# Optimization experiments

Measured on AMD Instinct MI355X. Metric: run time of the kernel, lower is better.

## Reference

```python
import jax, jax.numpy as jnp
import numpy as np

D_KEY = 128
INF = 1e9  # stands in for the module's global INF constant


def setup_inputs() -> dict:
    key = jax.random.key(0)
    kq, kk, kv = jax.random.split(key, 3)
    B, S, D = 8, 4096, D_KEY
    return {
        "query": jax.random.normal(kq, (B, S, D), dtype=jnp.float32),
        "keys": jax.random.normal(kk, (B, S, D), dtype=jnp.float32),
        "values": jax.random.normal(kv, (B, S, D), dtype=jnp.float32),
    }


def reference(query, keys, values):
    # dot_products: [B, Sq, Sk]
    scores = jnp.einsum("bqd,bkd->bqk", query, keys)
    S = scores.shape[-1]
    # causal: subtract INF on strict upper triangle (triu(1)), applied BEFORE scaling
    causal = jnp.triu(jnp.ones((S, S), dtype=scores.dtype), 1) * INF
    logits = (scores - causal[None, :, :]) / jnp.asarray(np.sqrt(D_KEY), scores.dtype)
    # legacy F.softmax on 3D transposed tensor == softmax over key axis
    probs = jax.nn.softmax(logits, axis=-1)
    # dropout with p=0.0 is identity
    return jnp.einsum("bqk,bkd->bqd", probs, values)
```

## Files before the change

### kernel.cpp

```cpp
#include <hip/hip_runtime.h>

#define B_SZ   8
#define S_LEN  4096
#define D_K    128
#define KB     64
#define CH     16
#define NCHUNK 1280

#define PT_STR 72

typedef short  short8  __attribute__((ext_vector_type(8)));
typedef float  floatx4 __attribute__((ext_vector_type(4)));

#define EXP2F(x) exp2f(x)

__device__ __forceinline__ unsigned bfround(float x) {
  unsigned u = __builtin_bit_cast(unsigned, x);
  return (u + 0x7fffu + ((u >> 16) & 1u)) >> 16;
}
__device__ __forceinline__ unsigned bfpack2(float a, float b) {
  return bfround(a) | (bfround(b) << 16);
}
__device__ __forceinline__ unsigned cvtpk(float lo, float hi) {
  unsigned r;
  asm("v_cvt_pk_bf16_f32 %0, %1, %2" : "=v"(r) : "v"(lo), "v"(hi));
  return r;
}

__device__ __forceinline__ void dma16(const void* g, const void* l) {
  __builtin_amdgcn_global_load_lds(
      (__attribute__((address_space(1))) unsigned int*)(unsigned long long)g,
      (__attribute__((address_space(3))) unsigned int*)(unsigned int)(unsigned long long)l,
      16, 0, 0);
}


__global__ __launch_bounds__(256)
void prep(const float* __restrict__ K, const float* __restrict__ V,
          unsigned short* __restrict__ Kb, unsigned short* __restrict__ Vt) {
  __shared__ float tile[64][129];
  const int tid = threadIdx.x;
  const int bid = blockIdx.x;
  const int b   = bid >> 6;
  const int s   = bid & 63;
  const int kt  = s * 64;

  {
    const int r  = tid >> 2;
    const int cq = tid & 3;
    const float* kp = K + (size_t)(b * S_LEN + kt + r) * D_K + cq * 32;
    unsigned short* kdst = Kb + (size_t)bid * 8192 + r * 128;
    const int xr = (r & 7) << 4;
#pragma unroll
    for (int j = 0; j < 4; ++j) {
      float4 f0 = *(const float4*)(kp + j * 8);
      float4 f1 = *(const float4*)(kp + j * 8 + 4);
      uint4 u;
      u.x = bfpack2(f0.x, f0.y);
      u.y = bfpack2(f0.z, f0.w);
      u.z = bfpack2(f1.x, f1.y);
      u.w = bfpack2(f1.z, f1.w);
      const int o = (cq * 64 + j * 16) ^ xr;
      *(uint4*)(kdst + (o >> 1)) = u;
    }
  }

  {
    const int k  = tid >> 2;
    const int cq = tid & 3;
    const float* vp = V + (size_t)(b * S_LEN + kt + k) * D_K + cq * 32;
#pragma unroll
    for (int i = 0; i < 8; ++i) {
      float4 f = *(const float4*)(vp + i * 4);
      tile[k][cq * 32 + i * 4]     = f.x;
      tile[k][cq * 32 + i * 4 + 1] = f.y;
      tile[k][cq * 32 + i * 4 + 2] = f.z;
      tile[k][cq * 32 + i * 4 + 3] = f.w;
    }
  }
  __syncthreads();

  {
    const int d = tid >> 1;
    const int h = tid & 1;
    unsigned short* vdst = Vt + (size_t)bid * 8192 + d * 64;
    const int xr = (d & 7) << 4;
#pragma unroll
    for (int j = 0; j < 4; ++j) {
      const int k0 = h * 32 + j * 8;
      uint4 u;
      u.x = bfpack2(tile[k0 + 0][d], tile[k0 + 1][d]);
      u.y = bfpack2(tile[k0 + 2][d], tile[k0 + 3][d]);
      u.z = bfpack2(tile[k0 + 4][d], tile[k0 + 5][d]);
      u.w = bfpack2(tile[k0 + 6][d], tile[k0 + 7][d]);
      const int o = (h * 64 + j * 16) ^ xr;
      *(uint4*)(vdst + (o >> 1)) = u;
    }
  }
}

__global__ void zero_cnt(int* cnt) { *cnt = 0; }


__global__ __launch_bounds__(128, 2)
void attn_worker(const float* __restrict__ Q, const unsigned short* __restrict__ Kb,
                 const unsigned short* __restrict__ Vt, int* __restrict__ cnt,
                 float* __restrict__ ml, float* __restrict__ pO) {
  __shared__ __align__(16) short Klds[2][8192];
  __shared__ __align__(16) short Vtlds[2][8192];
  __shared__ __align__(16) short Plds[2 * 16 * PT_STR];
  __shared__ int s_chunk;

  const int tid  = threadIdx.x;
  const int lane = tid & 63;
  const int w    = tid >> 6;
  const int l15  = lane & 15;
  const int quad = lane >> 4;
  const int xk   = (l15 & 7) << 3;

  const float CSC = 0.12752041f;

  for (;;) {
    if (tid == 0) s_chunk = atomicAdd(cnt, 1);
    __syncthreads();
    const int c = s_chunk;
    if (c >= NCHUNK) break;

    int b, qi, j;
    if (c < 800) {
      const int r = c >> 3;  b = c & 7;
      if      (r <  4) { qi = 63;               j = r;            }
      else if (r < 52) { qi = 62 - (r-4)/3;     j = (r-4)%3;      }
      else if (r < 84) { qi = 46 - (r-52)/2;    j = (r-52)%2;     }
      else             { qi = 30 - (r-84);      j = 0;            }
    } else {
      const int rc = c - 800;
      const int s  = 15 - (rc >> 5);
      const int t  = rc & 31;
      b  = t & 7;
      qi = s - 1 + 16 * (t >> 3);
      j  = (qi + 1) >> 4;
    }

    const int q0 = qi * 64;
    const int s0 = j * CH;
    const int s1 = min(s0 + CH, qi + 1);

    short8 bq[2][4];
    int qg[2];
#pragma unroll
    for (int sub = 0; sub < 2; ++sub) {
      qg[sub] = q0 + w * 32 + sub * 16 + l15;
      const float* qrow = Q + (size_t)(b * S_LEN + qg[sub]) * D_K + quad * 8;
#pragma unroll
      for (int kd = 0; kd < 4; ++kd) {
        float4 f0 = *(const float4*)(qrow + kd * 32);
        float4 f1 = *(const float4*)(qrow + kd * 32 + 4);
        union { short8 s; unsigned u[4]; } t;
        t.u[0] = bfpack2(f0.x, f0.y);
        t.u[1] = bfpack2(f0.z, f0.w);
        t.u[2] = bfpack2(f1.x, f1.y);
        t.u[3] = bfpack2(f1.z, f1.w);
        bq[sub][kd] = t.s;
      }
    }

    floatx4 acc[2][8];
#pragma unroll
    for (int sub = 0; sub < 2; ++sub)
#pragma unroll
      for (int nc = 0; nc < 8; ++nc) acc[sub][nc] = (floatx4){0.f, 0.f, 0.f, 0.f};
    float m_run[2] = {-1e30f, -1e30f}, l_run[2] = {0.f, 0.f};

    const unsigned short* kb0 = Kb + (size_t)b * 64 * 8192;
    const unsigned short* vb0 = Vt + (size_t)b * 64 * 8192;
    const int lo = lane * 8;

#define STAGE(BUF, S)                                                          \
    do {                                                                       \
      const unsigned short* kg_ = kb0 + (size_t)(S) * 8192 + w * 4096 + lo;    \
      const unsigned short* vg_ = vb0 + (size_t)(S) * 8192 + w * 4096 + lo;    \
      short* kl_ = &Klds[BUF][w * 4096];                                       \
      short* vl_ = &Vtlds[BUF][w * 4096];                                      \
      _Pragma("unroll")                                                        \
      for (int i_ = 0; i_ < 8; ++i_) dma16(kg_ + i_ * 512, kl_ + i_ * 512);    \
      _Pragma("unroll")                                                        \
      for (int i_ = 0; i_ < 8; ++i_) dma16(vg_ + i_ * 512, vl_ + i_ * 512);    \
    } while (0)

    STAGE(s0 & 1, s0);
    if (s0 + 1 < s1) {
      STAGE((s0 + 1) & 1, s0 + 1);
      asm volatile("s_waitcnt vmcnt(16)" ::: "memory");
    } else {
      asm volatile("s_waitcnt vmcnt(0)" ::: "memory");
    }
    __builtin_amdgcn_s_barrier();
    __builtin_amdgcn_sched_barrier(0);

    for (int s = s0; s < s1; ++s) {
      const int kt  = s * KB;
      const int cur = s & 1;
      const short* Kl = &Klds[cur][0];
      const short* Vl = &Vtlds[cur][0];

      floatx4 st[2][4];
#pragma unroll
      for (int kf = 0; kf < 4; ++kf) {
        floatx4 c0 = (floatx4){0.f, 0.f, 0.f, 0.f};
        floatx4 c1 = (floatx4){0.f, 0.f, 0.f, 0.f};
#pragma unroll
        for (int kd = 0; kd < 4; ++kd) {
          short8 a = *(const short8*)(&Kl[((kf * 16 + l15) << 7) + ((kd * 32 + quad * 8) ^ xk)]);
          c0 = __builtin_amdgcn_mfma_f32_16x16x32_bf16(a, bq[0][kd], c0, 0, 0, 0);
          c1 = __builtin_amdgcn_mfma_f32_16x16x32_bf16(a, bq[1][kd], c1, 0, 0, 0);
        }
        st[0][kf] = c0;
        st[1][kf] = c1;
      }

      if (s == qi) {
#pragma unroll
        for (int sub = 0; sub < 2; ++sub)
#pragma unroll
          for (int kf = 0; kf < 4; ++kf)
#pragma unroll
            for (int r = 0; r < 4; ++r) {
              int key = kt + kf * 16 + quad * 4 + r;
              if (key > qg[sub]) st[sub][kf][r] = -1e30f;
            }
      }

      short8 pa[2][2];
#pragma unroll
      for (int sub = 0; sub < 2; ++sub) {
        float mx = st[sub][0][0];
#pragma unroll
        for (int kf = 0; kf < 4; ++kf)
#pragma unroll
          for (int r = 0; r < 4; ++r) mx = fmaxf(mx, st[sub][kf][r]);
        mx = fmaxf(mx, __shfl_xor(mx, 16, 64));
        mx = fmaxf(mx, __shfl_xor(mx, 32, 64));
        const float m_new = fmaxf(m_run[sub], mx);
        const float alpha = EXP2F((m_run[sub] - m_new) * CSC);

        float p[4][4];
        float tsum = 0.f;
#pragma unroll
        for (int kf = 0; kf < 4; ++kf)
#pragma unroll
          for (int r = 0; r < 4; ++r) {
            p[kf][r] = EXP2F((st[sub][kf][r] - m_new) * CSC);
            tsum += p[kf][r];
          }
        tsum += __shfl_xor(tsum, 16, 64);
        tsum += __shfl_xor(tsum, 32, 64);
        l_run[sub] = l_run[sub] * alpha + tsum;
        m_run[sub] = m_new;

#pragma unroll
        for (int r = 0; r < 4; ++r) {
          const float ar = __shfl(alpha, quad * 4 + r, 64);
#pragma unroll
          for (int nc = 0; nc < 8; ++nc) acc[sub][nc][r] *= ar;
        }

        short* pw = &Plds[(w * 16 + l15) * PT_STR];
#pragma unroll
        for (int kf = 0; kf < 4; ++kf) {
          uint2 u;
          u.x = cvtpk(p[kf][0], p[kf][1]);
          u.y = cvtpk(p[kf][2], p[kf][3]);
          *(uint2*)(&pw[kf * 16 + quad * 4]) = u;
        }
        __asm__ __volatile__("" ::: "memory");
        pa[sub][0] = *(const short8*)(&pw[quad * 8]);
        pa[sub][1] = *(const short8*)(&pw[32 + quad * 8]);
        __asm__ __volatile__("" ::: "memory");
      }

#pragma unroll
      for (int nc = 0; nc < 8; ++nc) {
        short8 bv0 = *(const short8*)(&Vl[((nc * 16 + l15) << 6) + ((quad * 8) ^ xk)]);
        short8 bv1 = *(const short8*)(&Vl[((nc * 16 + l15) << 6) + ((32 + quad * 8) ^ xk)]);
        acc[0][nc] = __builtin_amdgcn_mfma_f32_16x16x32_bf16(pa[0][0], bv0, acc[0][nc], 0, 0, 0);
        acc[0][nc] = __builtin_amdgcn_mfma_f32_16x16x32_bf16(pa[0][1], bv1, acc[0][nc], 0, 0, 0);
        acc[1][nc] = __builtin_amdgcn_mfma_f32_16x16x32_bf16(pa[1][0], bv0, acc[1][nc], 0, 0, 0);
        acc[1][nc] = __builtin_amdgcn_mfma_f32_16x16x32_bf16(pa[1][1], bv1, acc[1][nc], 0, 0, 0);
      }

      asm volatile("s_waitcnt lgkmcnt(0)" ::: "memory");
      __builtin_amdgcn_s_barrier();
      __builtin_amdgcn_sched_barrier(0);
      if (s + 2 < s1) {
        STAGE(cur, s + 2);
        asm volatile("s_waitcnt vmcnt(16)" ::: "memory");
      } else if (s + 1 < s1) {
        asm volatile("s_waitcnt vmcnt(0)" ::: "memory");
      }
      __builtin_amdgcn_s_barrier();
      __builtin_amdgcn_sched_barrier(0);
    }
#undef STAGE

    const int slot = ((b << 6) | qi) * 4 + j;
    float* po = pO + (size_t)slot * 8192;
#pragma unroll
    for (int sub = 0; sub < 2; ++sub) {
#pragma unroll
      for (int r = 0; r < 4; ++r) {
        const int qrow = w * 32 + sub * 16 + quad * 4 + r;
        float* op = po + qrow * D_K + l15;
#pragma unroll
        for (int nc = 0; nc < 8; ++nc) op[nc * 16] = acc[sub][nc][r];
      }
      if (quad == 0) {
        const int qrow = w * 32 + sub * 16 + l15;
        ml[(size_t)slot * 128 + qrow * 2]     = m_run[sub];
        ml[(size_t)slot * 128 + qrow * 2 + 1] = l_run[sub];
      }
    }
  }
}


__global__ __launch_bounds__(256)
void attn_combine(const float* __restrict__ ml, const float* __restrict__ pO,
                  float* __restrict__ O) {
  const int t   = blockIdx.x;
  const int b   = t >> 6;
  const int qi  = t & 63;
  const int ncb = ((qi + 1) + 15) >> 4;
  const float CSC = 0.12752041f;

  const int tid = threadIdx.x;
  const int q   = tid >> 2;
  const int dp  = (tid & 3) * 32;

  float m[4], l[4];
  float M = -1e30f;
  for (int jj = 0; jj < ncb; ++jj) {
    const int slot = t * 4 + jj;
    m[jj] = ml[(size_t)slot * 128 + q * 2];
    l[jj] = ml[(size_t)slot * 128 + q * 2 + 1];
    M = fmaxf(M, m[jj]);
  }
  float wgt[4], L = 0.f;
  for (int jj = 0; jj < ncb; ++jj) {
    wgt[jj] = EXP2F((m[jj] - M) * CSC);
    L += wgt[jj] * l[jj];
  }
  const float inv = 1.0f / L;

  float4 out[8];
#pragma unroll
  for (int v = 0; v < 8; ++v) out[v] = make_float4(0.f, 0.f, 0.f, 0.f);
  for (int jj = 0; jj < ncb; ++jj) {
    const float* src = pO + (size_t)(t * 4 + jj) * 8192 + q * D_K + dp;
    const float wj = wgt[jj];
#pragma unroll
    for (int v = 0; v < 8; ++v) {
      float4 f = *(const float4*)(src + v * 4);
      out[v].x += wj * f.x;  out[v].y += wj * f.y;
      out[v].z += wj * f.z;  out[v].w += wj * f.w;
    }
  }
  float* dst = O + (size_t)(b * S_LEN + qi * 64 + q) * D_K + dp;
#pragma unroll
  for (int v = 0; v < 8; ++v) {
    float4 f = make_float4(out[v].x * inv, out[v].y * inv, out[v].z * inv, out[v].w * inv);
    *(float4*)(dst + v * 4) = f;
  }
}


#define KT_STR 136
#define VT_STR 72

__global__ __launch_bounds__(256, 2)
void attn_fwd_fb(const float* __restrict__ Q, const float* __restrict__ K,
                 const float* __restrict__ V, float* __restrict__ O) {
  __shared__ __align__(16) short Klds[KB * KT_STR];
  __shared__ __align__(16) short Vtlds[D_K * VT_STR];
  __shared__ __align__(16) short Plds[4 * 16 * PT_STR];

  const int tid  = threadIdx.x;
  const int lane = tid & 63;
  const int w    = tid >> 6;
  const int l15  = lane & 15;
  const int quad = lane >> 4;

  const int bid = blockIdx.x;
  const int b   = bid & 7;
  const int qi  = 63 - (bid >> 3);
  const int q0  = qi * 64;

  const float CSC = 0.12752041f;

  const int    qg   = q0 + w * 16 + l15;
  const float* qrow = Q + (size_t)(b * S_LEN + qg) * D_K + quad * 8;
  short8 bq[4];
#pragma unroll
  for (int kd = 0; kd < 4; ++kd) {
    float4 f0 = *(const float4*)(qrow + kd * 32);
    float4 f1 = *(const float4*)(qrow + kd * 32 + 4);
    union { short8 s; unsigned u[4]; } t;
    t.u[0] = bfpack2(f0.x, f0.y);
    t.u[1] = bfpack2(f0.z, f0.w);
    t.u[2] = bfpack2(f1.x, f1.y);
    t.u[3] = bfpack2(f1.z, f1.w);
    bq[kd] = t.s;
  }

  floatx4 acc[8];
#pragma unroll
  for (int nc = 0; nc < 8; ++nc) acc[nc] = (floatx4){0.f, 0.f, 0.f, 0.f};
  float m_run = -1e30f, l_run = 0.f;

  const int d4 = tid & 31;
  const int kq = tid >> 5;
  const int nsteps = qi + 1;

  for (int s = 0; s < nsteps; ++s) {
    const int kt = s * KB;
#pragma unroll
    for (int r2 = 0; r2 < 2; ++r2) {
      const int row = r2 * 32 + kq * 4;
      const float* kp = K + (size_t)(b * S_LEN + kt + row) * D_K + d4 * 4;
      const float* vp = V + (size_t)(b * S_LEN + kt + row) * D_K + d4 * 4;
      float4 fk[4], fv[4];
#pragma unroll
      for (int i = 0; i < 4; ++i) {
        fk[i] = *(const float4*)(kp + i * D_K);
        fv[i] = *(const float4*)(vp + i * D_K);
      }
#pragma unroll
      for (int i = 0; i < 4; ++i) {
        uint2 u;
        u.x = bfpack2(fk[i].x, fk[i].y);
        u.y = bfpack2(fk[i].z, fk[i].w);
        *(uint2*)(&Klds[(row + i) * KT_STR + d4 * 4]) = u;
      }
#pragma unroll
      for (int c = 0; c < 4; ++c) {
        float e0 = ((const float*)&fv[0])[c];
        float e1 = ((const float*)&fv[1])[c];
        float e2 = ((const float*)&fv[2])[c];
        float e3 = ((const float*)&fv[3])[c];
        uint2 u;
        u.x = bfpack2(e0, e1);
        u.y = bfpack2(e2, e3);
        *(uint2*)(&Vtlds[(d4 * 4 + c) * VT_STR + row]) = u;
      }
    }
    __syncthreads();

    floatx4 st[4];
#pragma unroll
    for (int kf = 0; kf < 4; ++kf) {
      floatx4 c = (floatx4){0.f, 0.f, 0.f, 0.f};
#pragma unroll
      for (int kd = 0; kd < 4; ++kd) {
        short8 a = *(const short8*)(&Klds[(kf * 16 + l15) * KT_STR + kd * 32 + quad * 8]);
        c = __builtin_amdgcn_mfma_f32_16x16x32_bf16(a, bq[kd], c, 0, 0, 0);
      }
      st[kf] = c;
    }

    if (s == nsteps - 1) {
#pragma unroll
      for (int kf = 0; kf < 4; ++kf)
#pragma unroll
        for (int rr = 0; rr < 4; ++rr) {
          int key = kt + kf * 16 + quad * 4 + rr;
          if (key > qg) st[kf][rr] = -1e30f;
        }
    }

    float mx = st[0][0];
#pragma unroll
    for (int kf = 0; kf < 4; ++kf)
#pragma unroll
      for (int rr = 0; rr < 4; ++rr) mx = fmaxf(mx, st[kf][rr]);
    mx = fmaxf(mx, __shfl_xor(mx, 16, 64));
    mx = fmaxf(mx, __shfl_xor(mx, 32, 64));
    const float m_new = fmaxf(m_run, mx);
    const float alpha = EXP2F((m_run - m_new) * CSC);

    float p[4][4];
    float tsum = 0.f;
#pragma unroll
    for (int kf = 0; kf < 4; ++kf)
#pragma unroll
      for (int rr = 0; rr < 4; ++rr) {
        p[kf][rr] = EXP2F((st[kf][rr] - m_new) * CSC);
        tsum += p[kf][rr];
      }
    tsum += __shfl_xor(tsum, 16, 64);
    tsum += __shfl_xor(tsum, 32, 64);
    l_run = l_run * alpha + tsum;
    m_run = m_new;

#pragma unroll
    for (int rr = 0; rr < 4; ++rr) {
      const float ar = __shfl(alpha, quad * 4 + rr, 64);
#pragma unroll
      for (int nc = 0; nc < 8; ++nc) acc[nc][rr] *= ar;
    }

    short* pw = &Plds[(w * 16 + l15) * PT_STR];
#pragma unroll
    for (int kf = 0; kf < 4; ++kf) {
      uint2 u;
      u.x = bfpack2(p[kf][0], p[kf][1]);
      u.y = bfpack2(p[kf][2], p[kf][3]);
      *(uint2*)(&pw[kf * 16 + quad * 4]) = u;
    }
    __asm__ __volatile__("" ::: "memory");
    short8 pa0 = *(const short8*)(&pw[quad * 8]);
    short8 pa1 = *(const short8*)(&pw[32 + quad * 8]);

#pragma unroll
    for (int nc = 0; nc < 8; ++nc) {
      short8 bv0 = *(const short8*)(&Vtlds[(nc * 16 + l15) * VT_STR + quad * 8]);
      acc[nc] = __builtin_amdgcn_mfma_f32_16x16x32_bf16(pa0, bv0, acc[nc], 0, 0, 0);
      short8 bv1 = *(const short8*)(&Vtlds[(nc * 16 + l15) * VT_STR + 32 + quad * 8]);
      acc[nc] = __builtin_amdgcn_mfma_f32_16x16x32_bf16(pa1, bv1, acc[nc], 0, 0, 0);
    }
    __syncthreads();
  }

#pragma unroll
  for (int rr = 0; rr < 4; ++rr) {
    const float lr  = __shfl(l_run, quad * 4 + rr, 64);
    const float inv = 1.0f / lr;
    const int qout  = q0 + w * 16 + quad * 4 + rr;
    float* op = O + (size_t)(b * S_LEN + qout) * D_K + l15;
#pragma unroll
    for (int nc = 0; nc < 8; ++nc) op[nc * 16] = acc[nc][rr] * inv;
  }
}


extern "C" void kernel_launch(void* const* d_in, const int* in_sizes, int n_in,
                              void* d_out, int out_size, void* d_ws, size_t ws_size,
                              hipStream_t stream) {
  const float* Q = (const float*)d_in[0];
  const float* K = (const float*)d_in[1];
  const float* V = (const float*)d_in[2];
  float* O = (float*)d_out;

  const size_t elems = (size_t)B_SZ * S_LEN * D_K;

  const size_t off_ml = 256;
  const size_t off_po = off_ml + 2048ull * 128 * 4;
  const size_t off_kb = off_po + 2048ull * 8192 * 4;
  const size_t off_vt = off_kb + elems * 2;
  const size_t need   = off_vt + elems * 2;

  if (ws_size >= need) {
    char* ws = (char*)d_ws;
    int*            cnt = (int*)ws;
    float*          mlp = (float*)(ws + off_ml);
    float*          po  = (float*)(ws + off_po);
    unsigned short* Kbp = (unsigned short*)(ws + off_kb);
    unsigned short* Vtp = (unsigned short*)(ws + off_vt);

    zero_cnt<<<dim3(1), dim3(1), 0, stream>>>(cnt);
    prep<<<dim3(B_SZ * 64), dim3(256), 0, stream>>>(K, V, Kbp, Vtp);
    attn_worker<<<dim3(1024), dim3(128), 0, stream>>>(Q, Kbp, Vtp, cnt, mlp, po);
    attn_combine<<<dim3(512), dim3(256), 0, stream>>>(mlp, po, O);
  } else {
    attn_fwd_fb<<<dim3(512), dim3(256), 0, stream>>>(Q, K, V, O);
  }
}
```

Baseline: 217.7 us.

## Use 128-row query tiles with 4-wave workgroups sharing each K/V stage

Doubles the query tile per work chunk from 64 to 128 rows, with four waves per workgroup instead of two. Each staged K/V block in LDS now serves twice as many queries, which halves the number of chunks and the global-to-LDS traffic per query. Waves whose rows lie entirely before the current key block skip their compute, and the causal mask is applied per 16-row sub-block. The combine kernel and workspace layout are resized to match; the coarser tiles reduce load-balancing granularity and add more idle waves along the diagonal.

```diff
diff --git a/kernel.cpp b/kernel.cpp
--- a/kernel.cpp
+++ b/kernel.cpp
@@ -5,7 +5,7 @@
 #define D_K    128
 #define KB     64
 #define CH     16
-#define NCHUNK 1280
+#define NCHUNK 640
 
 #define PT_STR 72
 
@@ -52,15 +52,15 @@
     unsigned short* kdst = Kb + (size_t)bid * 8192 + r * 128;
     const int xr = (r & 7) << 4;
 #pragma unroll
-    for (int j = 0; j < 4; ++j) {
-      float4 f0 = *(const float4*)(kp + j * 8);
-      float4 f1 = *(const float4*)(kp + j * 8 + 4);
+    for (int jj = 0; jj < 4; ++jj) {
+      float4 f0 = *(const float4*)(kp + jj * 8);
+      float4 f1 = *(const float4*)(kp + jj * 8 + 4);
       uint4 u;
       u.x = bfpack2(f0.x, f0.y);
       u.y = bfpack2(f0.z, f0.w);
       u.z = bfpack2(f1.x, f1.y);
       u.w = bfpack2(f1.z, f1.w);
-      const int o = (cq * 64 + j * 16) ^ xr;
+      const int o = (cq * 64 + jj * 16) ^ xr;
       *(uint4*)(kdst + (o >> 1)) = u;
     }
   }
@@ -86,14 +86,14 @@
     unsigned short* vdst = Vt + (size_t)bid * 8192 + d * 64;
     const int xr = (d & 7) << 4;
 #pragma unroll
-    for (int j = 0; j < 4; ++j) {
-      const int k0 = h * 32 + j * 8;
+    for (int jj = 0; jj < 4; ++jj) {
+      const int k0 = h * 32 + jj * 8;
       uint4 u;
       u.x = bfpack2(tile[k0 + 0][d], tile[k0 + 1][d]);
       u.y = bfpack2(tile[k0 + 2][d], tile[k0 + 3][d]);
       u.z = bfpack2(tile[k0 + 4][d], tile[k0 + 5][d]);
       u.w = bfpack2(tile[k0 + 6][d], tile[k0 + 7][d]);
-      const int o = (h * 64 + j * 16) ^ xr;
+      const int o = (h * 64 + jj * 16) ^ xr;
       *(uint4*)(vdst + (o >> 1)) = u;
     }
   }
@@ -102,13 +102,13 @@
 __global__ void zero_cnt(int* cnt) { *cnt = 0; }
 
 
-__global__ __launch_bounds__(128, 2)
+__global__ __launch_bounds__(256, 2)
 void attn_worker(const float* __restrict__ Q, const unsigned short* __restrict__ Kb,
                  const unsigned short* __restrict__ Vt, int* __restrict__ cnt,
                  float* __restrict__ ml, float* __restrict__ pO) {
   __shared__ __align__(16) short Klds[2][8192];
   __shared__ __align__(16) short Vtlds[2][8192];
-  __shared__ __align__(16) short Plds[2 * 16 * PT_STR];
+  __shared__ __align__(16) short Plds[4 * 16 * PT_STR];
   __shared__ int s_chunk;
 
   const int tid  = threadIdx.x;
@@ -126,25 +126,25 @@
     const int c = s_chunk;
     if (c >= NCHUNK) break;
 
-    int b, qi, j;
-    if (c < 800) {
+    int b, q, j;
+    if (c < 416) {
       const int r = c >> 3;  b = c & 7;
-      if      (r <  4) { qi = 63;               j = r;            }
-      else if (r < 52) { qi = 62 - (r-4)/3;     j = (r-4)%3;      }
-      else if (r < 84) { qi = 46 - (r-52)/2;    j = (r-52)%2;     }
-      else             { qi = 30 - (r-84);      j = 0;            }
+      if      (r <  4) { q = 31;              j = r;         }
+      else if (r < 28) { q = 30 - (r-4)/3;    j = (r-4)%3;   }
+      else if (r < 44) { q = 22 - (r-28)/2;   j = (r-28)%2;  }
+      else             { q = 14 - (r-44);     j = 0;         }
     } else {
-      const int rc = c - 800;
-      const int s  = 15 - (rc >> 5);
+      const int rc = c - 416;
+      const int g  = rc >> 5;
       const int t  = rc & 31;
-      b  = t & 7;
-      qi = s - 1 + 16 * (t >> 3);
-      j  = (qi + 1) >> 4;
-    }
-
-    const int q0 = qi * 64;
+      b = t & 7;
+      q = (6 - g) + 8 * (3 - (t >> 3));
+      j = (q + 1) >> 3;
+    }
+
+    const int q0 = q * 128;
     const int s0 = j * CH;
-    const int s1 = min(s0 + CH, qi + 1);
+    const int s1 = min(s0 + CH, 2 * q + 2);
 
     short8 bq[2][4];
     int qg[2];
@@ -178,20 +178,20 @@
 
 #define STAGE(BUF, S)                                                          \
     do {                                                                       \
-      const unsigned short* kg_ = kb0 + (size_t)(S) * 8192 + w * 4096 + lo;    \
-      const unsigned short* vg_ = vb0 + (size_t)(S) * 8192 + w * 4096 + lo;    \
-      short* kl_ = &Klds[BUF][w * 4096];                                       \
-      short* vl_ = &Vtlds[BUF][w * 4096];                                      \
+      const unsigned short* kg_ = kb0 + (size_t)(S) * 8192 + w * 2048 + lo;    \
+      const unsigned short* vg_ = vb0 + (size_t)(S) * 8192 + w * 2048 + lo;    \
+      short* kl_ = &Klds[BUF][w * 2048];                                       \
+      short* vl_ = &Vtlds[BUF][w * 2048];                                      \
       _Pragma("unroll")                                                        \
-      for (int i_ = 0; i_ < 8; ++i_) dma16(kg_ + i_ * 512, kl_ + i_ * 512);    \
+      for (int i_ = 0; i_ < 4; ++i_) dma16(kg_ + i_ * 512, kl_ + i_ * 512);    \
       _Pragma("unroll")                                                        \
-      for (int i_ = 0; i_ < 8; ++i_) dma16(vg_ + i_ * 512, vl_ + i_ * 512);    \
+      for (int i_ = 0; i_ < 4; ++i_) dma16(vg_ + i_ * 512, vl_ + i_ * 512);    \
     } while (0)
 
     STAGE(s0 & 1, s0);
     if (s0 + 1 < s1) {
       STAGE((s0 + 1) & 1, s0 + 1);
-      asm volatile("s_waitcnt vmcnt(16)" ::: "memory");
+      asm volatile("s_waitcnt vmcnt(8)" ::: "memory");
     } else {
       asm volatile("s_waitcnt vmcnt(0)" ::: "memory");
     }
@@ -203,90 +203,94 @@
       const int cur = s & 1;
       const short* Kl = &Klds[cur][0];
       const short* Vl = &Vtlds[cur][0];
-
-      floatx4 st[2][4];
-#pragma unroll
-      for (int kf = 0; kf < 4; ++kf) {
-        floatx4 c0 = (floatx4){0.f, 0.f, 0.f, 0.f};
-        floatx4 c1 = (floatx4){0.f, 0.f, 0.f, 0.f};
-#pragma unroll
-        for (int kd = 0; kd < 4; ++kd) {
-          short8 a = *(const short8*)(&Kl[((kf * 16 + l15) << 7) + ((kd * 32 + quad * 8) ^ xk)]);
-          c0 = __builtin_amdgcn_mfma_f32_16x16x32_bf16(a, bq[0][kd], c0, 0, 0, 0);
-          c1 = __builtin_amdgcn_mfma_f32_16x16x32_bf16(a, bq[1][kd], c1, 0, 0, 0);
+      const bool act = (kt <= q0 + w * 32 + 31);
+
+      short8 pa[2][2];
+      if (act) {
+        floatx4 st[2][4];
+#pragma unroll
+        for (int kf = 0; kf < 4; ++kf) {
+          floatx4 c0 = (floatx4){0.f, 0.f, 0.f, 0.f};
+          floatx4 c1 = (floatx4){0.f, 0.f, 0.f, 0.f};
+#pragma unroll
+          for (int kd = 0; kd < 4; ++kd) {
+            short8 a = *(const short8*)(&Kl[((kf * 16 + l15) << 7) + ((kd * 32 + quad * 8) ^ xk)]);
+            c0 = __builtin_amdgcn_mfma_f32_16x16x32_bf16(a, bq[0][kd], c0, 0, 0, 0);
+            c1 = __builtin_amdgcn_mfma_f32_16x16x32_bf16(a, bq[1][kd], c1, 0, 0, 0);
+          }
+          st[0][kf] = c0;
+          st[1][kf] = c1;
         }
-        st[0][kf] = c0;
-        st[1][kf] = c1;
-      }
-
-      if (s == qi) {
-#pragma unroll
-        for (int sub = 0; sub < 2; ++sub)
+
+#pragma unroll
+        for (int sub = 0; sub < 2; ++sub) {
+          if (kt + 63 > q0 + w * 32 + sub * 16) {
+#pragma unroll
+            for (int kf = 0; kf < 4; ++kf)
+#pragma unroll
+              for (int r = 0; r < 4; ++r) {
+                int key = kt + kf * 16 + quad * 4 + r;
+                if (key > qg[sub]) st[sub][kf][r] = -1e30f;
+              }
+          }
+        }
+
+#pragma unroll
+        for (int sub = 0; sub < 2; ++sub) {
+          float mx = st[sub][0][0];
 #pragma unroll
           for (int kf = 0; kf < 4; ++kf)
 #pragma unroll
+            for (int r = 0; r < 4; ++r) mx = fmaxf(mx, st[sub][kf][r]);
+          mx = fmaxf(mx, __shfl_xor(mx, 16, 64));
+          mx = fmaxf(mx, __shfl_xor(mx, 32, 64));
+          const float m_new = fmaxf(m_run[sub], mx);
+          const float alpha = EXP2F((m_run[sub] - m_new) * CSC);
+
+          float p[4][4];
+          float tsum = 0.f;
+#pragma unroll
+          for (int kf = 0; kf < 4; ++kf)
+#pragma unroll
             for (int r = 0; r < 4; ++r) {
-              int key = kt + kf * 16 + quad * 4 + r;
-              if (key > qg[sub]) st[sub][kf][r] = -1e30f;
+              p[kf][r] = EXP2F((st[sub][kf][r] - m_new) * CSC);
+              tsum += p[kf][r];
             }
-      }
-
-      short8 pa[2][2];
-#pragma unroll
-      for (int sub = 0; sub < 2; ++sub) {
-        float mx = st[sub][0][0];
-#pragma unroll
-        for (int kf = 0; kf < 4; ++kf)
-#pragma unroll
-          for (int r = 0; r < 4; ++r) mx = fmaxf(mx, st[sub][kf][r]);
-        mx = fmaxf(mx, __shfl_xor(mx, 16, 64));
-        mx = fmaxf(mx, __shfl_xor(mx, 32, 64));
-        const float m_new = fmaxf(m_run[sub], mx);
-        const float alpha = EXP2F((m_run[sub] - m_new) * CSC);
-
-        float p[4][4];
-        float tsum = 0.f;
-#pragma unroll
-        for (int kf = 0; kf < 4; ++kf)
+          tsum += __shfl_xor(tsum, 16, 64);
+          tsum += __shfl_xor(tsum, 32, 64);
+          l_run[sub] = l_run[sub] * alpha + tsum;
+          m_run[sub] = m_new;
+
 #pragma unroll
           for (int r = 0; r < 4; ++r) {
-            p[kf][r] = EXP2F((st[sub][kf][r] - m_new) * CSC);
-            tsum += p[kf][r];
+            const float ar = __shfl(alpha, quad * 4 + r, 64);
+#pragma unroll
+            for (int nc = 0; nc < 8; ++nc) acc[sub][nc][r] *= ar;
           }
-        tsum += __shfl_xor(tsum, 16, 64);
-        tsum += __shfl_xor(tsum, 32, 64);
-        l_run[sub] = l_run[sub] * alpha + tsum;
-        m_run[sub] = m_new;
-
-#pragma unroll
-        for (int r = 0; r < 4; ++r) {
-          const float ar = __shfl(alpha, quad * 4 + r, 64);
-#pragma unroll
-          for (int nc = 0; nc < 8; ++nc) acc[sub][nc][r] *= ar;
+
+          short* pw = &Plds[(w * 16 + l15) * PT_STR];
+#pragma unroll
+          for (int kf = 0; kf < 4; ++kf) {
+            uint2 u;
+            u.x = cvtpk(p[kf][0], p[kf][1]);
+            u.y = cvtpk(p[kf][2], p[kf][3]);
+            *(uint2*)(&pw[kf * 16 + quad * 4]) = u;
+          }
+          __asm__ __volatile__("" ::: "memory");
+          pa[sub][0] = *(const short8*)(&pw[quad * 8]);
+          pa[sub][1] = *(const short8*)(&pw[32 + quad * 8]);
+          __asm__ __volatile__("" ::: "memory");
         }
 
-        short* pw = &Plds[(w * 16 + l15) * PT_STR];
-#pragma unroll
-        for (int kf = 0; kf < 4; ++kf) {
-          uint2 u;
-          u.x = cvtpk(p[kf][0], p[kf][1]);
-          u.y = cvtpk(p[kf][2], p[kf][3]);
-          *(uint2*)(&pw[kf * 16 + quad * 4]) = u;
+#pragma unroll
+        for (int nc = 0; nc < 8; ++nc) {
+          short8 bv0 = *(const short8*)(&Vl[((nc * 16 + l15) << 6) + ((quad * 8) ^ xk)]);
+          short8 bv1 = *(const short8*)(&Vl[((nc * 16 + l15) << 6) + ((32 + quad * 8) ^ xk)]);
+          acc[0][nc] = __builtin_amdgcn_mfma_f32_16x16x32_bf16(pa[0][0], bv0, acc[0][nc], 0, 0, 0);
+          acc[0][nc] = __builtin_amdgcn_mfma_f32_16x16x32_bf16(pa[0][1], bv1, acc[0][nc], 0, 0, 0);
+          acc[1][nc] = __builtin_amdgcn_mfma_f32_16x16x32_bf16(pa[1][0], bv0, acc[1][nc], 0, 0, 0);
+          acc[1][nc] = __builtin_amdgcn_mfma_f32_16x16x32_bf16(pa[1][1], bv1, acc[1][nc], 0, 0, 0);
         }
-        __asm__ __volatile__("" ::: "memory");
-        pa[sub][0] = *(const short8*)(&pw[quad * 8]);
-        pa[sub][1] = *(const short8*)(&pw[32 + quad * 8]);
-        __asm__ __volatile__("" ::: "memory");
-      }
-
-#pragma unroll
-      for (int nc = 0; nc < 8; ++nc) {
-        short8 bv0 = *(const short8*)(&Vl[((nc * 16 + l15) << 6) + ((quad * 8) ^ xk)]);
-        short8 bv1 = *(const short8*)(&Vl[((nc * 16 + l15) << 6) + ((32 + quad * 8) ^ xk)]);
-        acc[0][nc] = __builtin_amdgcn_mfma_f32_16x16x32_bf16(pa[0][0], bv0, acc[0][nc], 0, 0, 0);
-        acc[0][nc] = __builtin_amdgcn_mfma_f32_16x16x32_bf16(pa[0][1], bv1, acc[0][nc], 0, 0, 0);
-        acc[1][nc] = __builtin_amdgcn_mfma_f32_16x16x32_bf16(pa[1][0], bv0, acc[1][nc], 0, 0, 0);
-        acc[1][nc] = __builtin_amdgcn_mfma_f32_16x16x32_bf16(pa[1][1], bv1, acc[1][nc], 0, 0, 0);
       }
 
       asm volatile("s_waitcnt lgkmcnt(0)" ::: "memory");
@@ -294,7 +298,7 @@
       __builtin_amdgcn_sched_barrier(0);
       if (s + 2 < s1) {
         STAGE(cur, s + 2);
-        asm volatile("s_waitcnt vmcnt(16)" ::: "memory");
+        asm volatile("s_waitcnt vmcnt(8)" ::: "memory");
       } else if (s + 1 < s1) {
         asm volatile("s_waitcnt vmcnt(0)" ::: "memory");
       }
@@ -303,8 +307,8 @@
     }
 #undef STAGE
 
-    const int slot = ((b << 6) | qi) * 4 + j;
-    float* po = pO + (size_t)slot * 8192;
+    const int slot = ((b << 5) | q) * 4 + j;
+    float* po = pO + (size_t)slot * 16384;
 #pragma unroll
     for (int sub = 0; sub < 2; ++sub) {
 #pragma unroll
@@ -316,8 +320,8 @@
       }
       if (quad == 0) {
         const int qrow = w * 32 + sub * 16 + l15;
-        ml[(size_t)slot * 128 + qrow * 2]     = m_run[sub];
-        ml[(size_t)slot * 128 + qrow * 2 + 1] = l_run[sub];
+        ml[(size_t)slot * 256 + qrow * 2]     = m_run[sub];
+        ml[(size_t)slot * 256 + qrow * 2 + 1] = l_run[sub];
       }
     }
   }
@@ -327,49 +331,54 @@
 __global__ __launch_bounds__(256)
 void attn_combine(const float* __restrict__ ml, const float* __restrict__ pO,
                   float* __restrict__ O) {
-  const int t   = blockIdx.x;
-  const int b   = t >> 6;
-  const int qi  = t & 63;
-  const int ncb = ((qi + 1) + 15) >> 4;
+  const int t = blockIdx.x;
+  const int b = t >> 5;
+  const int q = t & 31;
+  const int ncb = (2 * q + 17) >> 4;
   const float CSC = 0.12752041f;
 
   const int tid = threadIdx.x;
-  const int q   = tid >> 2;
-  const int dp  = (tid & 3) * 32;
-
-  float m[4], l[4];
+  const int ql  = tid >> 1;
+  const int dh  = (tid & 1) * 64;
+
+  float m[4], l[4], wgt[4];
   float M = -1e30f;
-  for (int jj = 0; jj < ncb; ++jj) {
-    const int slot = t * 4 + jj;
-    m[jj] = ml[(size_t)slot * 128 + q * 2];
-    l[jj] = ml[(size_t)slot * 128 + q * 2 + 1];
-    M = fmaxf(M, m[jj]);
-  }
-  float wgt[4], L = 0.f;
-  for (int jj = 0; jj < ncb; ++jj) {
-    wgt[jj] = EXP2F((m[jj] - M) * CSC);
-    L += wgt[jj] * l[jj];
-  }
+#pragma unroll
+  for (int jj = 0; jj < 4; ++jj) {
+    if (jj < ncb) {
+      const int slot = t * 4 + jj;
+      m[jj] = ml[(size_t)slot * 256 + ql * 2];
+      l[jj] = ml[(size_t)slot * 256 + ql * 2 + 1];
+      M = fmaxf(M, m[jj]);
+    }
+  }
+  float L = 0.f;
+#pragma unroll
+  for (int jj = 0; jj < 4; ++jj)
+    if (jj < ncb) { wgt[jj] = EXP2F((m[jj] - M) * CSC); L += wgt[jj] * l[jj]; }
   const float inv = 1.0f / L;
 
-  float4 out[8];
-#pragma unroll
-  for (int v = 0; v < 8; ++v) out[v] = make_float4(0.f, 0.f, 0.f, 0.f);
-  for (int jj = 0; jj < ncb; ++jj) {
-    const float* src = pO + (size_t)(t * 4 + jj) * 8192 + q * D_K + dp;
-    const float wj = wgt[jj];
-#pragma unroll
-    for (int v = 0; v < 8; ++v) {
-      float4 f = *(const float4*)(src + v * 4);
-      out[v].x += wj * f.x;  out[v].y += wj * f.y;
-      out[v].z += wj * f.z;  out[v].w += wj * f.w;
-    }
-  }
-  float* dst = O + (size_t)(b * S_LEN + qi * 64 + q) * D_K + dp;
-#pragma unroll
-  for (int v = 0; v < 8; ++v) {
-    float4 f = make_float4(out[v].x * inv, out[v].y * inv, out[v].z * inv, out[v].w * inv);
-    *(float4*)(dst + v * 4) = f;
+  float4 out[16];
+#pragma unroll
+  for (int v = 0; v < 16; ++v) out[v] = make_float4(0.f, 0.f, 0.f, 0.f);
+#pragma unroll
+  for (int jj = 0; jj < 4; ++jj) {
+    if (jj < ncb) {
+      const float* src = pO + (size_t)(t * 4 + jj) * 16384 + ql * D_K + dh;
+      const float wj = wgt[jj];
+#pragma unroll
+      for (int v = 0; v < 16; ++v) {
+        float4 f = *(const float4*)(src + v * 4);
+        out[v].x += wj * f.x;  out[v].y += wj * f.y;
+        out[v].z += wj * f.z;  out[v].w += wj * f.w;
+      }
+    }
+  }
+  float* dst = O + ((size_t)(b * S_LEN) + q * 128 + ql) * D_K + dh;
+#pragma unroll
+  for (int v = 0; v < 16; ++v) {
+    *(float4*)(dst + v * 4) = make_float4(out[v].x * inv, out[v].y * inv,
+                                          out[v].z * inv, out[v].w * inv);
   }
 }
 
@@ -458,13 +467,13 @@
     floatx4 st[4];
 #pragma unroll
     for (int kf = 0; kf < 4; ++kf) {
-      floatx4 c = (floatx4){0.f, 0.f, 0.f, 0.f};
+      floatx4 cc = (floatx4){0.f, 0.f, 0.f, 0.f};
 #pragma unroll
       for (int kd = 0; kd < 4; ++kd) {
         short8 a = *(const short8*)(&Klds[(kf * 16 + l15) * KT_STR + kd * 32 + quad * 8]);
-        c = __builtin_amdgcn_mfma_f32_16x16x32_bf16(a, bq[kd], c, 0, 0, 0);
-      }
-      st[kf] = c;
+        cc = __builtin_amdgcn_mfma_f32_16x16x32_bf16(a, bq[kd], cc, 0, 0, 0);
+      }
+      st[kf] = cc;
     }
 
     if (s == nsteps - 1) {
@@ -553,8 +562,8 @@
   const size_t elems = (size_t)B_SZ * S_LEN * D_K;
 
   const size_t off_ml = 256;
-  const size_t off_po = off_ml + 2048ull * 128 * 4;
-  const size_t off_kb = off_po + 2048ull * 8192 * 4;
+  const size_t off_po = off_ml + 1024ull * 256 * 4;
+  const size_t off_kb = off_po + 1024ull * 16384 * 4;
   const size_t off_vt = off_kb + elems * 2;
   const size_t need   = off_vt + elems * 2;
 
@@ -568,8 +577,8 @@
 
     zero_cnt<<<dim3(1), dim3(1), 0, stream>>>(cnt);
     prep<<<dim3(B_SZ * 64), dim3(256), 0, stream>>>(K, V, Kbp, Vtp);
-    attn_worker<<<dim3(1024), dim3(128), 0, stream>>>(Q, Kbp, Vtp, cnt, mlp, po);
-    attn_combine<<<dim3(512), dim3(256), 0, stream>>>(mlp, po, O);
+    attn_worker<<<dim3(512), dim3(256), 0, stream>>>(Q, Kbp, Vtp, cnt, mlp, po);
+    attn_combine<<<dim3(256), dim3(256), 0, stream>>>(mlp, po, O);
   } else {
     attn_fwd_fb<<<dim3(512), dim3(256), 0, stream>>>(Q, K, V, O);
   }
```

Result: faster. 187.6 us (-13.8%).
